# Kernel tuning notes

Hardware: AMD Instinct MI355X
Metric: run time of the kernel (lower is better)

## Reference

```python
import jax, jax.numpy as jnp
import numpy as np

B, T, D_MODEL, N_HEADS, D_HEAD = 2, 2048, 1024, 16, 64


def apply_rotary_emb(x, cos, sin):
    # x: [B, H, T, Dh]; cos, sin: [T, Dh//2]. Interleaved-pair RoPE.
    x1 = x[..., 0::2]  # [B,H,T,Dh/2]
    x2 = x[..., 1::2]
    c = cos[None, None, :, :]
    s = sin[None, None, :, :]
    out_even = x1 * c - x2 * s
    out_odd = x1 * s + x2 * c
    return jnp.stack([out_even, out_odd], axis=-1).reshape(x.shape)


def setup_inputs() -> dict:
    key = jax.random.key(0)
    ks = jax.random.split(key, 7)
    x = jax.random.normal(ks[0], (B, T, D_MODEL), dtype=jnp.float32)
    cos = jax.random.uniform(ks[1], (T, D_HEAD // 2), dtype=jnp.float32)
    sin = jax.random.uniform(ks[2], (T, D_HEAD // 2), dtype=jnp.float32)
    scale = 1.0 / np.sqrt(D_MODEL)
    W_q = jax.random.normal(ks[3], (D_MODEL, N_HEADS * D_HEAD), dtype=jnp.float32) * scale
    W_k = jax.random.normal(ks[4], (D_MODEL, N_HEADS * D_HEAD), dtype=jnp.float32) * scale
    W_v = jax.random.normal(ks[5], (D_MODEL, N_HEADS * D_HEAD), dtype=jnp.float32) * scale
    W_out = jax.random.normal(ks[6], (N_HEADS * D_HEAD, D_MODEL), dtype=jnp.float32) * scale
    return {"x": x, "cos": cos, "sin": sin, "W_q": W_q, "W_k": W_k, "W_v": W_v, "W_out": W_out}


def reference(x, cos, sin, W_q, W_k, W_v, W_out):
    Bb, Tt, _ = x.shape
    q = (x @ W_q).reshape(Bb, Tt, N_HEADS, D_HEAD).transpose(0, 2, 1, 3)  # [B,H,T,Dh]
    k = (x @ W_k).reshape(Bb, Tt, N_HEADS, D_HEAD).transpose(0, 2, 1, 3)
    v = (x @ W_v).reshape(Bb, Tt, N_HEADS, D_HEAD).transpose(0, 2, 1, 3)
    q = apply_rotary_emb(q, cos, sin)
    k = apply_rotary_emb(k, cos, sin)
    scores = jnp.einsum('bhqd,bhkd->bhqk', q, k) / np.sqrt(D_HEAD).astype(np.float32)
    causal = jnp.tril(jnp.ones((Tt, Tt), dtype=bool))
    scores = jnp.where(causal[None, None], scores, -jnp.inf)
    attn = jax.nn.softmax(scores, axis=-1)
    z = jnp.einsum('bhqk,bhkd->bhqd', attn, v)          # [B,H,T,Dh]
    z = z.transpose(0, 2, 1, 3).reshape(Bb, Tt, N_HEADS * D_HEAD)
    return z @ W_out
```

## Files before the change

### kernel.cpp

```cpp
#include <hip/hip_runtime.h>
#include <math.h>

#define TSEQ   2048
#define DMODEL 1024
#define NHEADS 16
#define DHEAD  64
#define BATCH  2

typedef __attribute__((ext_vector_type(8))) short short8;
typedef __attribute__((ext_vector_type(4))) float f32x4;

__device__ __forceinline__ unsigned short f2bf(float x) {
    union { float f; unsigned int u; } c; c.f = x;
    unsigned int r = (c.u + 0x7FFFu + ((c.u >> 16) & 1u)) >> 16;
    return (unsigned short)r;
}
__device__ __forceinline__ float bf2f(unsigned short h) {
    union { unsigned int u; float f; } c; c.u = ((unsigned int)h) << 16;
    return c.f;
}

__global__ __launch_bounds__(256) void qkv_rope_kernel(
    const float* __restrict__ x,
    const float* __restrict__ Wq, const float* __restrict__ Wk,
    const float* __restrict__ Wv,
    const float* __restrict__ cosb, const float* __restrict__ sinb,
    unsigned short* __restrict__ qhi, unsigned short* __restrict__ qlo,
    unsigned short* __restrict__ khi, unsigned short* __restrict__ klo,
    unsigned short* __restrict__ vto)
{
    __shared__ float As[16][132];
    __shared__ float Bs[16][132];

    const int tid = threadIdx.x;
    const int m0  = blockIdx.y * 128;
    const int n0g = blockIdx.x * 128;
    const int section = n0g >> 10;
    const int n0 = n0g & 1023;
    const float* __restrict__ W = (section == 0) ? Wq : (section == 1) ? Wk : Wv;

    const int arow = tid >> 2;
    const int ak   = (tid & 3) << 2;
    const int brow = tid >> 5;
    const int bn   = (tid & 31) << 2;

    const int rr = (tid & 15) << 2;
    const int cc = (tid >> 4) << 2;

    float acc[2][2][4][4] = {};

    const float* Aptr0 = x + (size_t)(m0 + arow) * DMODEL + ak;
    const float* Aptr1 = Aptr0 + (size_t)64 * DMODEL;
    const float* Bptr0 = W + (size_t)brow * DMODEL + n0 + bn;
    const float* Bptr1 = Bptr0 + (size_t)8 * DMODEL;

    float4 av0 = *(const float4*)(Aptr0);
    float4 av1 = *(const float4*)(Aptr1);
    float4 bv0 = *(const float4*)(Bptr0);
    float4 bv1 = *(const float4*)(Bptr1);

    for (int k0 = 0; k0 < DMODEL; k0 += 16) {
        __syncthreads();
        As[ak + 0][arow] = av0.x;  As[ak + 1][arow] = av0.y;
        As[ak + 2][arow] = av0.z;  As[ak + 3][arow] = av0.w;
        As[ak + 0][arow + 64] = av1.x;  As[ak + 1][arow + 64] = av1.y;
        As[ak + 2][arow + 64] = av1.z;  As[ak + 3][arow + 64] = av1.w;
        *(float4*)&Bs[brow][bn]     = bv0;
        *(float4*)&Bs[brow + 8][bn] = bv1;
        __syncthreads();
        if (k0 + 16 < DMODEL) {
            av0 = *(const float4*)(Aptr0 + k0 + 16);
            av1 = *(const float4*)(Aptr1 + k0 + 16);
            bv0 = *(const float4*)(Bptr0 + (size_t)(k0 + 16) * DMODEL);
            bv1 = *(const float4*)(Bptr1 + (size_t)(k0 + 16) * DMODEL);
        }
        #pragma unroll
        for (int kk = 0; kk < 16; ++kk) {
            float4 a0 = *(const float4*)&As[kk][rr];
            float4 a1 = *(const float4*)&As[kk][rr + 64];
            float4 b0 = *(const float4*)&Bs[kk][cc];
            float4 b1 = *(const float4*)&Bs[kk][cc + 64];
            float ar[2][4] = {{a0.x, a0.y, a0.z, a0.w}, {a1.x, a1.y, a1.z, a1.w}};
            float br[2][4] = {{b0.x, b0.y, b0.z, b0.w}, {b1.x, b1.y, b1.z, b1.w}};
            #pragma unroll
            for (int bi = 0; bi < 2; ++bi)
                #pragma unroll
                for (int i = 0; i < 4; ++i)
                    #pragma unroll
                    for (int bj = 0; bj < 2; ++bj)
                        #pragma unroll
                        for (int jj = 0; jj < 4; ++jj)
                            acc[bi][bj][i][jj] += ar[bi][i] * br[bj][jj];
        }
    }

    const int b = m0 >> 11;
    #pragma unroll
    for (int bi = 0; bi < 2; ++bi) {
        #pragma unroll
        for (int i = 0; i < 4; ++i) {
            const int t = (m0 + bi * 64 + rr + i) & (TSEQ - 1);
            #pragma unroll
            for (int bj = 0; bj < 2; ++bj) {
                const int n  = n0 + bj * 64 + cc;
                const int h  = n >> 6;
                const int d0 = n & 63;
                float a0 = acc[bi][bj][i][0], a1 = acc[bi][bj][i][1];
                float a2 = acc[bi][bj][i][2], a3 = acc[bi][bj][i][3];
                if (section < 2) {
                    const int p0 = d0 >> 1;
                    float c0v = cosb[t * (DHEAD / 2) + p0];
                    float s0v = sinb[t * (DHEAD / 2) + p0];
                    float c1v = cosb[t * (DHEAD / 2) + p0 + 1];
                    float s1v = sinb[t * (DHEAD / 2) + p0 + 1];
                    float r[4];
                    r[0] = a0 * c0v - a1 * s0v;
                    r[1] = a0 * s0v + a1 * c0v;
                    r[2] = a2 * c1v - a3 * s1v;
                    r[3] = a2 * s1v + a3 * c1v;
                    ushort4 uh, ul;
                    uh.x = f2bf(r[0]); ul.x = f2bf(r[0] - bf2f(uh.x));
                    uh.y = f2bf(r[1]); ul.y = f2bf(r[1] - bf2f(uh.y));
                    uh.z = f2bf(r[2]); ul.z = f2bf(r[2] - bf2f(uh.z));
                    uh.w = f2bf(r[3]); ul.w = f2bf(r[3] - bf2f(uh.w));
                    unsigned short* ph = (section == 0) ? qhi : khi;
                    unsigned short* pl = (section == 0) ? qlo : klo;
                    const size_t off = (((size_t)b * NHEADS + h) * TSEQ + t) * DHEAD + d0;
                    *(ushort4*)&ph[off] = uh;
                    *(ushort4*)&pl[off] = ul;
                } else {
                    const size_t base = ((size_t)b * NHEADS + h) * DHEAD;
                    vto[(base + d0 + 0) * TSEQ + t] = f2bf(a0);
                    vto[(base + d0 + 1) * TSEQ + t] = f2bf(a1);
                    vto[(base + d0 + 2) * TSEQ + t] = f2bf(a2);
                    vto[(base + d0 + 3) * TSEQ + t] = f2bf(a3);
                }
            }
        }
    }
}

#define LDSOFF(r, c) (((r) << 7) + ((((c) ^ ((r) & 7))) << 4))

__device__ __forceinline__ void stage64x64(const unsigned short* __restrict__ g,
                                           int rs_elems, char* lbase, int tid) {
    const int r = tid >> 3;
    const int c = tid & 7;
    const char* gb = (const char*)g;
    uint4 v0 = *(const uint4*)(gb + (size_t)r * rs_elems * 2 + (c << 4));
    uint4 v1 = *(const uint4*)(gb + (size_t)(r + 32) * rs_elems * 2 + (c << 4));
    *(uint4*)(lbase + LDSOFF(r, c)) = v0;
    *(uint4*)(lbase + LDSOFF(r + 32, c)) = v1;
}

__device__ __forceinline__ short8 frag(const char* lbase, int row, int chunk) {
    union { uint4 u; short8 s; } cv;
    cv.u = *(const uint4*)(lbase + LDSOFF(row, chunk));
    return cv.s;
}

__global__ __launch_bounds__(256) void attn_mfma_kernel(
    const unsigned short* __restrict__ qhig, const unsigned short* __restrict__ qlog,
    const unsigned short* __restrict__ khig, const unsigned short* __restrict__ klog,
    const unsigned short* __restrict__ vtg, float* __restrict__ z)
{
    __shared__ __align__(16) char smem[49152];
    char* Qhb = smem;
    char* Qlb = smem + 8192;
    char* Khb = smem + 16384;
    char* Klb = smem + 24576;
    char* Vb  = smem + 32768;
    char* Pb  = smem + 40960;

    const int tid  = threadIdx.x;
    const int lane = tid & 63;
    const int wave = tid >> 6;
    const int ln15 = lane & 15;
    const int g    = lane >> 4;

    const int bh = blockIdx.y;
    const int b  = bh >> 4;
    const int h  = bh & 15;
    const unsigned short* qhh = qhig + (size_t)bh * TSEQ * DHEAD;
    const unsigned short* qlh = qlog + (size_t)bh * TSEQ * DHEAD;
    const unsigned short* khh = khig + (size_t)bh * TSEQ * DHEAD;
    const unsigned short* klh = klog + (size_t)bh * TSEQ * DHEAD;
    const unsigned short* vth = vtg  + (size_t)bh * DHEAD * TSEQ;

    for (int half = 0; half < 2; ++half) {
        const int qt = half ? (31 - (int)blockIdx.x) : (int)blockIdx.x;

        __syncthreads();
        stage64x64(qhh + (size_t)qt * 64 * DHEAD, DHEAD, Qhb, tid);
        stage64x64(qlh + (size_t)qt * 64 * DHEAD, DHEAD, Qlb, tid);
        __syncthreads();

        const int rA = 16 * wave + ln15;
        short8 qh0 = frag(Qhb, rA, g),     qh1 = frag(Qhb, rA, 4 + g);
        short8 ql0 = frag(Qlb, rA, g),     ql1 = frag(Qlb, rA, 4 + g);

        float m_i[4], l_i[4];
        f32x4 oacc[4];
        #pragma unroll
        for (int i2 = 0; i2 < 4; ++i2) {
            m_i[i2] = -INFINITY; l_i[i2] = 0.f;
            oacc[i2][0] = 0.f; oacc[i2][1] = 0.f; oacc[i2][2] = 0.f; oacc[i2][3] = 0.f;
        }

        for (int jt = 0; jt <= qt; ++jt) {
            __syncthreads();
            stage64x64(khh + (size_t)jt * 64 * DHEAD, DHEAD, Khb, tid);
            stage64x64(klh + (size_t)jt * 64 * DHEAD, DHEAD, Klb, tid);
            stage64x64(vth + (size_t)jt * 64, TSEQ, Vb, tid);
            __syncthreads();

            f32x4 sacc[4];
            #pragma unroll
            for (int ct = 0; ct < 4; ++ct) {
                const int rB = ct * 16 + ln15;
                short8 kh0 = frag(Khb, rB, g), kh1 = frag(Khb, rB, 4 + g);
                short8 kl0 = frag(Klb, rB, g), kl1 = frag(Klb, rB, 4 + g);
                f32x4 acc = {0.f, 0.f, 0.f, 0.f};
                acc = __builtin_amdgcn_mfma_f32_16x16x32_bf16(qh0, kh0, acc, 0, 0, 0);
                acc = __builtin_amdgcn_mfma_f32_16x16x32_bf16(qh1, kh1, acc, 0, 0, 0);
                acc = __builtin_amdgcn_mfma_f32_16x16x32_bf16(qh0, kl0, acc, 0, 0, 0);
                acc = __builtin_amdgcn_mfma_f32_16x16x32_bf16(qh1, kl1, acc, 0, 0, 0);
                acc = __builtin_amdgcn_mfma_f32_16x16x32_bf16(ql0, kh0, acc, 0, 0, 0);
                acc = __builtin_amdgcn_mfma_f32_16x16x32_bf16(ql1, kh1, acc, 0, 0, 0);
                sacc[ct] = acc;
            }

            const bool diag = (jt == qt);
            #pragma unroll
            for (int reg = 0; reg < 4; ++reg) {
                const int rloc = 16 * wave + 4 * g + reg;
                float sv[4];
                #pragma unroll
                for (int ct = 0; ct < 4; ++ct) {
                    float xv = sacc[ct][reg] * 0.125f;
                    if (diag && (ct * 16 + ln15 > rloc)) xv = -INFINITY;
                    sv[ct] = xv;
                }
                float mr = fmaxf(fmaxf(sv[0], sv[1]), fmaxf(sv[2], sv[3]));
                #pragma unroll
                for (int off = 1; off < 16; off <<= 1)
                    mr = fmaxf(mr, __shfl_xor(mr, off));
                float mnew = fmaxf(m_i[reg], mr);
                float al   = __expf(m_i[reg] - mnew);
                float rs = 0.f;
                unsigned short pb[4];
                #pragma unroll
                for (int ct = 0; ct < 4; ++ct) {
                    float p = __expf(sv[ct] - mnew);
                    pb[ct] = f2bf(p);
                    rs += bf2f(pb[ct]);
                }
                #pragma unroll
                for (int off = 1; off < 16; off <<= 1)
                    rs += __shfl_xor(rs, off);
                l_i[reg] = l_i[reg] * al + rs;
                m_i[reg] = mnew;
                #pragma unroll
                for (int dt = 0; dt < 4; ++dt)
                    oacc[dt][reg] *= al;
                #pragma unroll
                for (int ct = 0; ct < 4; ++ct) {
                    const int col = ct * 16 + ln15;
                    const int chunk = col >> 3;
                    const int byt = (rloc << 7) + ((chunk ^ (rloc & 7)) << 4) + ((col & 7) << 1);
                    *(unsigned short*)(Pb + byt) = pb[ct];
                }
            }

            short8 pa0 = frag(Pb, rA, g);
            short8 pa1 = frag(Pb, rA, 4 + g);
            #pragma unroll
            for (int dt = 0; dt < 4; ++dt) {
                short8 vb0 = frag(Vb, dt * 16 + ln15, g);
                short8 vb1 = frag(Vb, dt * 16 + ln15, 4 + g);
                oacc[dt] = __builtin_amdgcn_mfma_f32_16x16x32_bf16(pa0, vb0, oacc[dt], 0, 0, 0);
                oacc[dt] = __builtin_amdgcn_mfma_f32_16x16x32_bf16(pa1, vb1, oacc[dt], 0, 0, 0);
            }
        }

        #pragma unroll
        for (int reg = 0; reg < 4; ++reg) {
            const float inv = 1.0f / l_i[reg];
            const int t = qt * 64 + 16 * wave + 4 * g + reg;
            float* zrow = z + ((size_t)(b * TSEQ + t)) * DMODEL + h * DHEAD;
            #pragma unroll
            for (int dt = 0; dt < 4; ++dt)
                zrow[dt * 16 + ln15] = oacc[dt][reg] * inv;
        }
    }
}

__global__ __launch_bounds__(256) void out_proj_kernel(
    const float* __restrict__ A, const float* __restrict__ B,
    float* __restrict__ C)
{
    __shared__ float As[16][132];
    __shared__ float Bs[16][132];

    const int tid = threadIdx.x;
    const int m0 = blockIdx.y * 128;
    const int n0 = blockIdx.x * 128;

    const int arow = tid >> 2;
    const int ak   = (tid & 3) << 2;
    const int brow = tid >> 5;
    const int bn   = (tid & 31) << 2;
    const int rr   = (tid & 15) << 2;
    const int cc   = (tid >> 4) << 2;

    float acc[2][2][4][4] = {};

    const float* Aptr0 = A + (size_t)(m0 + arow) * DMODEL + ak;
    const float* Aptr1 = Aptr0 + (size_t)64 * DMODEL;
    const float* Bptr0 = B + (size_t)brow * DMODEL + n0 + bn;
    const float* Bptr1 = Bptr0 + (size_t)8 * DMODEL;

    float4 av0 = *(const float4*)(Aptr0);
    float4 av1 = *(const float4*)(Aptr1);
    float4 bv0 = *(const float4*)(Bptr0);
    float4 bv1 = *(const float4*)(Bptr1);

    for (int k0 = 0; k0 < DMODEL; k0 += 16) {
        __syncthreads();
        As[ak + 0][arow] = av0.x;  As[ak + 1][arow] = av0.y;
        As[ak + 2][arow] = av0.z;  As[ak + 3][arow] = av0.w;
        As[ak + 0][arow + 64] = av1.x;  As[ak + 1][arow + 64] = av1.y;
        As[ak + 2][arow + 64] = av1.z;  As[ak + 3][arow + 64] = av1.w;
        *(float4*)&Bs[brow][bn]     = bv0;
        *(float4*)&Bs[brow + 8][bn] = bv1;
        __syncthreads();
        if (k0 + 16 < DMODEL) {
            av0 = *(const float4*)(Aptr0 + k0 + 16);
            av1 = *(const float4*)(Aptr1 + k0 + 16);
            bv0 = *(const float4*)(Bptr0 + (size_t)(k0 + 16) * DMODEL);
            bv1 = *(const float4*)(Bptr1 + (size_t)(k0 + 16) * DMODEL);
        }
        #pragma unroll
        for (int kk = 0; kk < 16; ++kk) {
            float4 a0 = *(const float4*)&As[kk][rr];
            float4 a1 = *(const float4*)&As[kk][rr + 64];
            float4 b0 = *(const float4*)&Bs[kk][cc];
            float4 b1 = *(const float4*)&Bs[kk][cc + 64];
            float ar[2][4] = {{a0.x, a0.y, a0.z, a0.w}, {a1.x, a1.y, a1.z, a1.w}};
            float br[2][4] = {{b0.x, b0.y, b0.z, b0.w}, {b1.x, b1.y, b1.z, b1.w}};
            #pragma unroll
            for (int bi = 0; bi < 2; ++bi)
                #pragma unroll
                for (int i = 0; i < 4; ++i)
                    #pragma unroll
                    for (int bj = 0; bj < 2; ++bj)
                        #pragma unroll
                        for (int jj = 0; jj < 4; ++jj)
                            acc[bi][bj][i][jj] += ar[bi][i] * br[bj][jj];
        }
    }

    #pragma unroll
    for (int bi = 0; bi < 2; ++bi)
        #pragma unroll
        for (int i = 0; i < 4; ++i) {
            const size_t row = m0 + bi * 64 + rr + i;
            #pragma unroll
            for (int bj = 0; bj < 2; ++bj) {
                const int col = n0 + bj * 64 + cc;
                *(float4*)&C[row * DMODEL + col] =
                    make_float4(acc[bi][bj][i][0], acc[bi][bj][i][1],
                                acc[bi][bj][i][2], acc[bi][bj][i][3]);
            }
        }
}

extern "C" void kernel_launch(void* const* d_in, const int* in_sizes, int n_in,
                              void* d_out, int out_size, void* d_ws, size_t ws_size,
                              hipStream_t stream)
{
    const float* x    = (const float*)d_in[0];
    const float* cosb = (const float*)d_in[1];
    const float* sinb = (const float*)d_in[2];
    const float* Wq   = (const float*)d_in[3];
    const float* Wk   = (const float*)d_in[4];
    const float* Wv   = (const float*)d_in[5];
    const float* Wo   = (const float*)d_in[6];
    float* out = (float*)d_out;

    const size_t per = (size_t)BATCH * NHEADS * TSEQ * DHEAD;
    unsigned short* qhi = (unsigned short*)d_ws;
    unsigned short* qlo = qhi + per;
    unsigned short* khi = qlo + per;
    unsigned short* klo = khi + per;
    unsigned short* vt  = klo + per;
    float* z = (float*)(vt + per);

    qkv_rope_kernel<<<dim3(24, 32), 256, 0, stream>>>(x, Wq, Wk, Wv, cosb, sinb,
                                                      qhi, qlo, khi, klo, vt);
    attn_mfma_kernel<<<dim3(16, 32), 256, 0, stream>>>(qhi, qlo, khi, klo, vt, z);
    out_proj_kernel<<<dim3(8, 32), 256, 0, stream>>>(z, Wo, out);
}
```

Baseline: 584.2 us.

## Move QKV and output projections to split-bf16 MFMA GEMMs with prep kernel

Adds a prep kernel that splits x and transposed weights into hi/lo bf16 pairs. The FP32 SIMT QKV and output-projection GEMMs are replaced with MFMA GEMMs that use three bf16 products to keep near-fp32 accuracy. Attention now writes z as a hi/lo split so the output projection can consume it directly. The trade is an extra prep pass over all four weight matrices on every call, plus a larger workspace, with a fallback to the old path when the workspace is too small.

```diff
diff --git a/kernel.cpp b/kernel.cpp
--- a/kernel.cpp
+++ b/kernel.cpp
@@ -19,8 +19,433 @@
     union { unsigned int u; float f; } c; c.u = ((unsigned int)h) << 16;
     return c.f;
 }
-
-__global__ __launch_bounds__(256) void qkv_rope_kernel(
+__device__ __forceinline__ void split2(float x, unsigned short& h, unsigned short& l) {
+    h = f2bf(x);
+    l = f2bf(x - bf2f(h));
+}
+
+__global__ __launch_bounds__(256) void prep_kernel(
+    const float* __restrict__ x,
+    const float* __restrict__ Wq, const float* __restrict__ Wk,
+    const float* __restrict__ Wv, const float* __restrict__ Wo,
+    unsigned short* __restrict__ xhi, unsigned short* __restrict__ xlo,
+    unsigned short* __restrict__ wth, unsigned short* __restrict__ wtl)
+{
+    const int tid = threadIdx.x;
+    const int bid = blockIdx.x;
+    if (bid < 1024) {
+        const size_t base = (size_t)bid * 4096;
+        #pragma unroll
+        for (int i = 0; i < 4; ++i) {
+            const size_t idx = base + (size_t)i * 1024 + tid * 4;
+            float4 v = *(const float4*)(x + idx);
+            ushort4 h4, l4;
+            split2(v.x, h4.x, l4.x); split2(v.y, h4.y, l4.y);
+            split2(v.z, h4.z, l4.z); split2(v.w, h4.w, l4.w);
+            *(ushort4*)(xhi + idx) = h4;
+            *(ushort4*)(xlo + idx) = l4;
+        }
+    } else {
+        __shared__ float tile[64][65];
+        const int tv = bid - 1024;
+        const int w  = tv >> 8;
+        const int kt = (tv & 255) >> 4;
+        const int nt = tv & 15;
+        const int k0 = kt * 64, n0 = nt * 64;
+        const float* __restrict__ W = (w == 0) ? Wq : (w == 1) ? Wk : (w == 2) ? Wv : Wo;
+        const int r = tid >> 4;
+        const int c = (tid & 15) * 4;
+        #pragma unroll
+        for (int i = 0; i < 4; ++i) {
+            float4 v = *(const float4*)(W + (size_t)(k0 + r + 16 * i) * DMODEL + n0 + c);
+            tile[r + 16 * i][c + 0] = v.x;
+            tile[r + 16 * i][c + 1] = v.y;
+            tile[r + 16 * i][c + 2] = v.z;
+            tile[r + 16 * i][c + 3] = v.w;
+        }
+        __syncthreads();
+        unsigned short* oh = wth + (size_t)w * DMODEL * DMODEL;
+        unsigned short* ol = wtl + (size_t)w * DMODEL * DMODEL;
+        #pragma unroll
+        for (int i = 0; i < 4; ++i) {
+            const int a = r + 16 * i;
+            ushort4 h4, l4;
+            split2(tile[c + 0][a], h4.x, l4.x);
+            split2(tile[c + 1][a], h4.y, l4.y);
+            split2(tile[c + 2][a], h4.z, l4.z);
+            split2(tile[c + 3][a], h4.w, l4.w);
+            const size_t off = (size_t)(n0 + a) * DMODEL + k0 + c;
+            *(ushort4*)(oh + off) = h4;
+            *(ushort4*)(ol + off) = l4;
+        }
+    }
+}
+
+#define LOFF4(r, ch) (((r) << 6) + ((((ch) ^ ((r) & 3))) << 4))
+
+__device__ __forceinline__ short8 frag4(const char* lb, int row, int ch) {
+    union { uint4 u; short8 s; } cv;
+    cv.u = *(const uint4*)(lb + LOFF4(row, ch));
+    return cv.s;
+}
+
+#define GEMM_STAGE_DECLS \
+    const int sr = tid >> 1;    \
+    const int shalf = tid & 1;  \
+    uint4 ra[2], rla[2], rb[2], rlb[2];
+
+#define GEMM_LOAD(kk) { \
+    const size_t ao = (size_t)arowg * DMODEL + (kk) + shalf * 16; \
+    ra[0]  = *(const uint4*)(Ahg + ao);  ra[1]  = *(const uint4*)(Ahg + ao + 8); \
+    rla[0] = *(const uint4*)(Alg + ao);  rla[1] = *(const uint4*)(Alg + ao + 8); \
+    const size_t bo = (size_t)browg * DMODEL + (kk) + shalf * 16; \
+    rb[0]  = *(const uint4*)(Bhg + bo);  rb[1]  = *(const uint4*)(Bhg + bo + 8); \
+    rlb[0] = *(const uint4*)(Blg + bo);  rlb[1] = *(const uint4*)(Blg + bo + 8); }
+
+#define GEMM_WRITE_LDS { \
+    *(uint4*)(Ah + LOFF4(sr, shalf * 2))     = ra[0]; \
+    *(uint4*)(Ah + LOFF4(sr, shalf * 2 + 1)) = ra[1]; \
+    *(uint4*)(Al + LOFF4(sr, shalf * 2))     = rla[0]; \
+    *(uint4*)(Al + LOFF4(sr, shalf * 2 + 1)) = rla[1]; \
+    *(uint4*)(Bh + LOFF4(sr, shalf * 2))     = rb[0]; \
+    *(uint4*)(Bh + LOFF4(sr, shalf * 2 + 1)) = rb[1]; \
+    *(uint4*)(Bl + LOFF4(sr, shalf * 2))     = rlb[0]; \
+    *(uint4*)(Bl + LOFF4(sr, shalf * 2 + 1)) = rlb[1]; }
+
+#define GEMM_COMPUTE { \
+    short8 fa[4], fla[4], fb[4], flb[4]; \
+    _Pragma("unroll") \
+    for (int mi = 0; mi < 4; ++mi) { \
+        fa[mi]  = frag4(Ah, wr * 64 + mi * 16 + ln15, g); \
+        fla[mi] = frag4(Al, wr * 64 + mi * 16 + ln15, g); \
+    } \
+    _Pragma("unroll") \
+    for (int nj = 0; nj < 4; ++nj) { \
+        fb[nj]  = frag4(Bh, wc * 64 + nj * 16 + ln15, g); \
+        flb[nj] = frag4(Bl, wc * 64 + nj * 16 + ln15, g); \
+    } \
+    _Pragma("unroll") \
+    for (int mi = 0; mi < 4; ++mi) \
+        _Pragma("unroll") \
+        for (int nj = 0; nj < 4; ++nj) { \
+            acc[mi][nj] = __builtin_amdgcn_mfma_f32_16x16x32_bf16(fa[mi],  fb[nj],  acc[mi][nj], 0, 0, 0); \
+            acc[mi][nj] = __builtin_amdgcn_mfma_f32_16x16x32_bf16(fa[mi],  flb[nj], acc[mi][nj], 0, 0, 0); \
+            acc[mi][nj] = __builtin_amdgcn_mfma_f32_16x16x32_bf16(fla[mi], fb[nj],  acc[mi][nj], 0, 0, 0); \
+        } }
+
+__global__ __launch_bounds__(256, 2) void qkv_mfma_kernel(
+    const unsigned short* __restrict__ xhi, const unsigned short* __restrict__ xlo,
+    const unsigned short* __restrict__ wth, const unsigned short* __restrict__ wtl,
+    const float* __restrict__ cosb, const float* __restrict__ sinb,
+    unsigned short* __restrict__ qhi, unsigned short* __restrict__ qlo,
+    unsigned short* __restrict__ khi, unsigned short* __restrict__ klo,
+    unsigned short* __restrict__ vto)
+{
+    __shared__ __align__(16) char smem[32768];
+    char* Ah = smem;
+    char* Al = smem + 8192;
+    char* Bh = smem + 16384;
+    char* Bl = smem + 24576;
+
+    const int tid  = threadIdx.x;
+    const int lane = tid & 63;
+    const int wave = tid >> 6;
+    const int ln15 = lane & 15;
+    const int g    = lane >> 4;
+    const int wr   = wave >> 1;
+    const int wc   = wave & 1;
+
+    const int m0    = blockIdx.y * 128;
+    const int sec   = blockIdx.x >> 3;
+    const int nsec0 = (blockIdx.x & 7) * 128;
+
+    const unsigned short* Ahg = xhi;
+    const unsigned short* Alg = xlo;
+    const unsigned short* Bhg = wth + (size_t)sec * DMODEL * DMODEL;
+    const unsigned short* Blg = wtl + (size_t)sec * DMODEL * DMODEL;
+
+    GEMM_STAGE_DECLS
+    const int arowg = m0 + sr;
+    const int browg = nsec0 + sr;
+
+    f32x4 acc[4][4];
+    #pragma unroll
+    for (int mi = 0; mi < 4; ++mi)
+        #pragma unroll
+        for (int nj = 0; nj < 4; ++nj)
+            acc[mi][nj] = (f32x4){0.f, 0.f, 0.f, 0.f};
+
+    GEMM_LOAD(0)
+    for (int k0 = 0; k0 < DMODEL; k0 += 32) {
+        __syncthreads();
+        GEMM_WRITE_LDS
+        __syncthreads();
+        if (k0 + 32 < DMODEL) GEMM_LOAD(k0 + 32)
+        GEMM_COMPUTE
+    }
+
+    unsigned short* oh = (sec == 0) ? qhi : khi;
+    unsigned short* ol = (sec == 0) ? qlo : klo;
+    #pragma unroll
+    for (int mi = 0; mi < 4; ++mi) {
+        #pragma unroll
+        for (int nj = 0; nj < 4; ++nj) {
+            const int colh = nsec0 + wc * 64 + nj * 16 + ln15;
+            const int h = colh >> 6;
+            const int d = colh & 63;
+            const int p = d >> 1;
+            const float sgn = (d & 1) ? 1.f : -1.f;
+            #pragma unroll
+            for (int reg = 0; reg < 4; ++reg) {
+                const int row = m0 + wr * 64 + mi * 16 + g * 4 + reg;
+                const int t = row & (TSEQ - 1);
+                const int b = row >> 11;
+                float v = acc[mi][nj][reg];
+                if (sec < 2) {
+                    float pv = __shfl_xor(v, 1);
+                    float cv = cosb[t * (DHEAD / 2) + p];
+                    float sv = sinb[t * (DHEAD / 2) + p];
+                    float rv = v * cv + pv * sv * sgn;
+                    unsigned short hh, ll;
+                    split2(rv, hh, ll);
+                    const size_t off = (((size_t)b * NHEADS + h) * TSEQ + t) * DHEAD + d;
+                    oh[off] = hh;
+                    ol[off] = ll;
+                } else {
+                    vto[(((size_t)b * NHEADS + h) * DHEAD + d) * TSEQ + t] = f2bf(v);
+                }
+            }
+        }
+    }
+}
+
+#define LDSOFF(r, c) (((r) << 7) + ((((c) ^ ((r) & 7))) << 4))
+
+__device__ __forceinline__ void stage64x64(const unsigned short* __restrict__ gm,
+                                           int rs_elems, char* lbase, int tid) {
+    const int r = tid >> 3;
+    const int c = tid & 7;
+    const char* gb = (const char*)gm;
+    uint4 v0 = *(const uint4*)(gb + (size_t)r * rs_elems * 2 + (c << 4));
+    uint4 v1 = *(const uint4*)(gb + (size_t)(r + 32) * rs_elems * 2 + (c << 4));
+    *(uint4*)(lbase + LDSOFF(r, c)) = v0;
+    *(uint4*)(lbase + LDSOFF(r + 32, c)) = v1;
+}
+
+__device__ __forceinline__ short8 frag(const char* lbase, int row, int chunk) {
+    union { uint4 u; short8 s; } cv;
+    cv.u = *(const uint4*)(lbase + LDSOFF(row, chunk));
+    return cv.s;
+}
+
+template<bool SPLITZ>
+__global__ __launch_bounds__(256) void attn_mfma_kernel(
+    const unsigned short* __restrict__ qhig, const unsigned short* __restrict__ qlog,
+    const unsigned short* __restrict__ khig, const unsigned short* __restrict__ klog,
+    const unsigned short* __restrict__ vtg,
+    float* __restrict__ zf,
+    unsigned short* __restrict__ zhi, unsigned short* __restrict__ zlo)
+{
+    __shared__ __align__(16) char smem[49152];
+    char* Qhb = smem;
+    char* Qlb = smem + 8192;
+    char* Khb = smem + 16384;
+    char* Klb = smem + 24576;
+    char* Vb  = smem + 32768;
+    char* Pb  = smem + 40960;
+
+    const int tid  = threadIdx.x;
+    const int lane = tid & 63;
+    const int wave = tid >> 6;
+    const int ln15 = lane & 15;
+    const int g    = lane >> 4;
+
+    const int bh = blockIdx.y;
+    const int b  = bh >> 4;
+    const int h  = bh & 15;
+    const unsigned short* qhh = qhig + (size_t)bh * TSEQ * DHEAD;
+    const unsigned short* qlh = qlog + (size_t)bh * TSEQ * DHEAD;
+    const unsigned short* khh = khig + (size_t)bh * TSEQ * DHEAD;
+    const unsigned short* klh = klog + (size_t)bh * TSEQ * DHEAD;
+    const unsigned short* vth = vtg  + (size_t)bh * DHEAD * TSEQ;
+
+    for (int half = 0; half < 2; ++half) {
+        const int qt = half ? (31 - (int)blockIdx.x) : (int)blockIdx.x;
+
+        __syncthreads();
+        stage64x64(qhh + (size_t)qt * 64 * DHEAD, DHEAD, Qhb, tid);
+        stage64x64(qlh + (size_t)qt * 64 * DHEAD, DHEAD, Qlb, tid);
+        __syncthreads();
+
+        const int rA = 16 * wave + ln15;
+        short8 qh0 = frag(Qhb, rA, g),     qh1 = frag(Qhb, rA, 4 + g);
+        short8 ql0 = frag(Qlb, rA, g),     ql1 = frag(Qlb, rA, 4 + g);
+
+        float m_i[4], l_i[4];
+        f32x4 oacc[4];
+        #pragma unroll
+        for (int i2 = 0; i2 < 4; ++i2) {
+            m_i[i2] = -INFINITY; l_i[i2] = 0.f;
+            oacc[i2][0] = 0.f; oacc[i2][1] = 0.f; oacc[i2][2] = 0.f; oacc[i2][3] = 0.f;
+        }
+
+        for (int jt = 0; jt <= qt; ++jt) {
+            __syncthreads();
+            stage64x64(khh + (size_t)jt * 64 * DHEAD, DHEAD, Khb, tid);
+            stage64x64(klh + (size_t)jt * 64 * DHEAD, DHEAD, Klb, tid);
+            stage64x64(vth + (size_t)jt * 64, TSEQ, Vb, tid);
+            __syncthreads();
+
+            f32x4 sacc[4];
+            #pragma unroll
+            for (int ct = 0; ct < 4; ++ct) {
+                const int rB = ct * 16 + ln15;
+                short8 kh0 = frag(Khb, rB, g), kh1 = frag(Khb, rB, 4 + g);
+                short8 kl0 = frag(Klb, rB, g), kl1 = frag(Klb, rB, 4 + g);
+                f32x4 a2 = {0.f, 0.f, 0.f, 0.f};
+                a2 = __builtin_amdgcn_mfma_f32_16x16x32_bf16(qh0, kh0, a2, 0, 0, 0);
+                a2 = __builtin_amdgcn_mfma_f32_16x16x32_bf16(qh1, kh1, a2, 0, 0, 0);
+                a2 = __builtin_amdgcn_mfma_f32_16x16x32_bf16(qh0, kl0, a2, 0, 0, 0);
+                a2 = __builtin_amdgcn_mfma_f32_16x16x32_bf16(qh1, kl1, a2, 0, 0, 0);
+                a2 = __builtin_amdgcn_mfma_f32_16x16x32_bf16(ql0, kh0, a2, 0, 0, 0);
+                a2 = __builtin_amdgcn_mfma_f32_16x16x32_bf16(ql1, kh1, a2, 0, 0, 0);
+                sacc[ct] = a2;
+            }
+
+            const bool diag = (jt == qt);
+            #pragma unroll
+            for (int reg = 0; reg < 4; ++reg) {
+                const int rloc = 16 * wave + 4 * g + reg;
+                float sv[4];
+                #pragma unroll
+                for (int ct = 0; ct < 4; ++ct) {
+                    float xv = sacc[ct][reg] * 0.125f;
+                    if (diag && (ct * 16 + ln15 > rloc)) xv = -INFINITY;
+                    sv[ct] = xv;
+                }
+                float mr = fmaxf(fmaxf(sv[0], sv[1]), fmaxf(sv[2], sv[3]));
+                #pragma unroll
+                for (int off = 1; off < 16; off <<= 1)
+                    mr = fmaxf(mr, __shfl_xor(mr, off));
+                float mnew = fmaxf(m_i[reg], mr);
+                float al   = __expf(m_i[reg] - mnew);
+                float rs = 0.f;
+                unsigned short pb[4];
+                #pragma unroll
+                for (int ct = 0; ct < 4; ++ct) {
+                    float pp = __expf(sv[ct] - mnew);
+                    pb[ct] = f2bf(pp);
+                    rs += bf2f(pb[ct]);
+                }
+                #pragma unroll
+                for (int off = 1; off < 16; off <<= 1)
+                    rs += __shfl_xor(rs, off);
+                l_i[reg] = l_i[reg] * al + rs;
+                m_i[reg] = mnew;
+                #pragma unroll
+                for (int dt = 0; dt < 4; ++dt)
+                    oacc[dt][reg] *= al;
+                #pragma unroll
+                for (int ct = 0; ct < 4; ++ct) {
+                    const int col = ct * 16 + ln15;
+                    const int chunk = col >> 3;
+                    const int byt = (rloc << 7) + ((chunk ^ (rloc & 7)) << 4) + ((col & 7) << 1);
+                    *(unsigned short*)(Pb + byt) = pb[ct];
+                }
+            }
+
+            short8 pa0 = frag(Pb, rA, g);
+            short8 pa1 = frag(Pb, rA, 4 + g);
+            #pragma unroll
+            for (int dt = 0; dt < 4; ++dt) {
+                short8 vb0 = frag(Vb, dt * 16 + ln15, g);
+                short8 vb1 = frag(Vb, dt * 16 + ln15, 4 + g);
+                oacc[dt] = __builtin_amdgcn_mfma_f32_16x16x32_bf16(pa0, vb0, oacc[dt], 0, 0, 0);
+                oacc[dt] = __builtin_amdgcn_mfma_f32_16x16x32_bf16(pa1, vb1, oacc[dt], 0, 0, 0);
+            }
+        }
+
+        #pragma unroll
+        for (int reg = 0; reg < 4; ++reg) {
+            const float inv = 1.0f / l_i[reg];
+            const int t = qt * 64 + 16 * wave + 4 * g + reg;
+            const size_t idx = ((size_t)(b * TSEQ + t)) * DMODEL + h * DHEAD;
+            #pragma unroll
+            for (int dt = 0; dt < 4; ++dt) {
+                float val = oacc[dt][reg] * inv;
+                if (SPLITZ) {
+                    unsigned short hh = f2bf(val);
+                    zhi[idx + dt * 16 + ln15] = hh;
+                    zlo[idx + dt * 16 + ln15] = f2bf(val - bf2f(hh));
+                } else {
+                    zf[idx + dt * 16 + ln15] = val;
+                }
+            }
+        }
+    }
+}
+
+__global__ __launch_bounds__(256, 2) void out_proj_mfma_kernel(
+    const unsigned short* __restrict__ zhi, const unsigned short* __restrict__ zlo,
+    const unsigned short* __restrict__ wth, const unsigned short* __restrict__ wtl,
+    float* __restrict__ outp)
+{
+    __shared__ __align__(16) char smem[32768];
+    char* Ah = smem;
+    char* Al = smem + 8192;
+    char* Bh = smem + 16384;
+    char* Bl = smem + 24576;
+
+    const int tid  = threadIdx.x;
+    const int lane = tid & 63;
+    const int wave = tid >> 6;
+    const int ln15 = lane & 15;
+    const int g    = lane >> 4;
+    const int wr   = wave >> 1;
+    const int wc   = wave & 1;
+
+    const int m0 = blockIdx.y * 128;
+    const int n0 = blockIdx.x * 128;
+
+    const unsigned short* Ahg = zhi;
+    const unsigned short* Alg = zlo;
+    const unsigned short* Bhg = wth + (size_t)3 * DMODEL * DMODEL;
+    const unsigned short* Blg = wtl + (size_t)3 * DMODEL * DMODEL;
+
+    GEMM_STAGE_DECLS
+    const int arowg = m0 + sr;
+    const int browg = n0 + sr;
+
+    f32x4 acc[4][4];
+    #pragma unroll
+    for (int mi = 0; mi < 4; ++mi)
+        #pragma unroll
+        for (int nj = 0; nj < 4; ++nj)
+            acc[mi][nj] = (f32x4){0.f, 0.f, 0.f, 0.f};
+
+    GEMM_LOAD(0)
+    for (int k0 = 0; k0 < DMODEL; k0 += 32) {
+        __syncthreads();
+        GEMM_WRITE_LDS
+        __syncthreads();
+        if (k0 + 32 < DMODEL) GEMM_LOAD(k0 + 32)
+        GEMM_COMPUTE
+    }
+
+    #pragma unroll
+    for (int mi = 0; mi < 4; ++mi)
+        #pragma unroll
+        for (int nj = 0; nj < 4; ++nj) {
+            const int col = n0 + wc * 64 + nj * 16 + ln15;
+            #pragma unroll
+            for (int reg = 0; reg < 4; ++reg) {
+                const int row = m0 + wr * 64 + mi * 16 + g * 4 + reg;
+                outp[(size_t)row * DMODEL + col] = acc[mi][nj][reg];
+            }
+        }
+}
+
+__global__ __launch_bounds__(256) void qkv_rope_f32_kernel(
     const float* __restrict__ x,
     const float* __restrict__ Wq, const float* __restrict__ Wk,
     const float* __restrict__ Wv,
@@ -43,7 +468,6 @@
     const int ak   = (tid & 3) << 2;
     const int brow = tid >> 5;
     const int bn   = (tid & 31) << 2;
-
     const int rr = (tid & 15) << 2;
     const int cc = (tid >> 4) << 2;
 
@@ -119,10 +543,10 @@
                     r[2] = a2 * c1v - a3 * s1v;
                     r[3] = a2 * s1v + a3 * c1v;
                     ushort4 uh, ul;
-                    uh.x = f2bf(r[0]); ul.x = f2bf(r[0] - bf2f(uh.x));
-                    uh.y = f2bf(r[1]); ul.y = f2bf(r[1] - bf2f(uh.y));
-                    uh.z = f2bf(r[2]); ul.z = f2bf(r[2] - bf2f(uh.z));
-                    uh.w = f2bf(r[3]); ul.w = f2bf(r[3] - bf2f(uh.w));
+                    split2(r[0], uh.x, ul.x);
+                    split2(r[1], uh.y, ul.y);
+                    split2(r[2], uh.z, ul.z);
+                    split2(r[3], uh.w, ul.w);
                     unsigned short* ph = (section == 0) ? qhi : khi;
                     unsigned short* pl = (section == 0) ? qlo : klo;
                     const size_t off = (((size_t)b * NHEADS + h) * TSEQ + t) * DHEAD + d0;
@@ -140,162 +564,7 @@
     }
 }
 
-#define LDSOFF(r, c) (((r) << 7) + ((((c) ^ ((r) & 7))) << 4))
-
-__device__ __forceinline__ void stage64x64(const unsigned short* __restrict__ g,
-                                           int rs_elems, char* lbase, int tid) {
-    const int r = tid >> 3;
-    const int c = tid & 7;
-    const char* gb = (const char*)g;
-    uint4 v0 = *(const uint4*)(gb + (size_t)r * rs_elems * 2 + (c << 4));
-    uint4 v1 = *(const uint4*)(gb + (size_t)(r + 32) * rs_elems * 2 + (c << 4));
-    *(uint4*)(lbase + LDSOFF(r, c)) = v0;
-    *(uint4*)(lbase + LDSOFF(r + 32, c)) = v1;
-}
-
-__device__ __forceinline__ short8 frag(const char* lbase, int row, int chunk) {
-    union { uint4 u; short8 s; } cv;
-    cv.u = *(const uint4*)(lbase + LDSOFF(row, chunk));
-    return cv.s;
-}
-
-__global__ __launch_bounds__(256) void attn_mfma_kernel(
-    const unsigned short* __restrict__ qhig, const unsigned short* __restrict__ qlog,
-    const unsigned short* __restrict__ khig, const unsigned short* __restrict__ klog,
-    const unsigned short* __restrict__ vtg, float* __restrict__ z)
-{
-    __shared__ __align__(16) char smem[49152];
-    char* Qhb = smem;
-    char* Qlb = smem + 8192;
-    char* Khb = smem + 16384;
-    char* Klb = smem + 24576;
-    char* Vb  = smem + 32768;
-    char* Pb  = smem + 40960;
-
-    const int tid  = threadIdx.x;
-    const int lane = tid & 63;
-    const int wave = tid >> 6;
-    const int ln15 = lane & 15;
-    const int g    = lane >> 4;
-
-    const int bh = blockIdx.y;
-    const int b  = bh >> 4;
-    const int h  = bh & 15;
-    const unsigned short* qhh = qhig + (size_t)bh * TSEQ * DHEAD;
-    const unsigned short* qlh = qlog + (size_t)bh * TSEQ * DHEAD;
-    const unsigned short* khh = khig + (size_t)bh * TSEQ * DHEAD;
-    const unsigned short* klh = klog + (size_t)bh * TSEQ * DHEAD;
-    const unsigned short* vth = vtg  + (size_t)bh * DHEAD * TSEQ;
-
-    for (int half = 0; half < 2; ++half) {
-        const int qt = half ? (31 - (int)blockIdx.x) : (int)blockIdx.x;
-
-        __syncthreads();
-        stage64x64(qhh + (size_t)qt * 64 * DHEAD, DHEAD, Qhb, tid);
-        stage64x64(qlh + (size_t)qt * 64 * DHEAD, DHEAD, Qlb, tid);
-        __syncthreads();
-
-        const int rA = 16 * wave + ln15;
-        short8 qh0 = frag(Qhb, rA, g),     qh1 = frag(Qhb, rA, 4 + g);
-        short8 ql0 = frag(Qlb, rA, g),     ql1 = frag(Qlb, rA, 4 + g);
-
-        float m_i[4], l_i[4];
-        f32x4 oacc[4];
-        #pragma unroll
-        for (int i2 = 0; i2 < 4; ++i2) {
-            m_i[i2] = -INFINITY; l_i[i2] = 0.f;
-            oacc[i2][0] = 0.f; oacc[i2][1] = 0.f; oacc[i2][2] = 0.f; oacc[i2][3] = 0.f;
-        }
-
-        for (int jt = 0; jt <= qt; ++jt) {
-            __syncthreads();
-            stage64x64(khh + (size_t)jt * 64 * DHEAD, DHEAD, Khb, tid);
-            stage64x64(klh + (size_t)jt * 64 * DHEAD, DHEAD, Klb, tid);
-            stage64x64(vth + (size_t)jt * 64, TSEQ, Vb, tid);
-            __syncthreads();
-
-            f32x4 sacc[4];
-            #pragma unroll
-            for (int ct = 0; ct < 4; ++ct) {
-                const int rB = ct * 16 + ln15;
-                short8 kh0 = frag(Khb, rB, g), kh1 = frag(Khb, rB, 4 + g);
-                short8 kl0 = frag(Klb, rB, g), kl1 = frag(Klb, rB, 4 + g);
-                f32x4 acc = {0.f, 0.f, 0.f, 0.f};
-                acc = __builtin_amdgcn_mfma_f32_16x16x32_bf16(qh0, kh0, acc, 0, 0, 0);
-                acc = __builtin_amdgcn_mfma_f32_16x16x32_bf16(qh1, kh1, acc, 0, 0, 0);
-                acc = __builtin_amdgcn_mfma_f32_16x16x32_bf16(qh0, kl0, acc, 0, 0, 0);
-                acc = __builtin_amdgcn_mfma_f32_16x16x32_bf16(qh1, kl1, acc, 0, 0, 0);
-                acc = __builtin_amdgcn_mfma_f32_16x16x32_bf16(ql0, kh0, acc, 0, 0, 0);
-                acc = __builtin_amdgcn_mfma_f32_16x16x32_bf16(ql1, kh1, acc, 0, 0, 0);
-                sacc[ct] = acc;
-            }
-
-            const bool diag = (jt == qt);
-            #pragma unroll
-            for (int reg = 0; reg < 4; ++reg) {
-                const int rloc = 16 * wave + 4 * g + reg;
-                float sv[4];
-                #pragma unroll
-                for (int ct = 0; ct < 4; ++ct) {
-                    float xv = sacc[ct][reg] * 0.125f;
-                    if (diag && (ct * 16 + ln15 > rloc)) xv = -INFINITY;
-                    sv[ct] = xv;
-                }
-                float mr = fmaxf(fmaxf(sv[0], sv[1]), fmaxf(sv[2], sv[3]));
-                #pragma unroll
-                for (int off = 1; off < 16; off <<= 1)
-                    mr = fmaxf(mr, __shfl_xor(mr, off));
-                float mnew = fmaxf(m_i[reg], mr);
-                float al   = __expf(m_i[reg] - mnew);
-                float rs = 0.f;
-                unsigned short pb[4];
-                #pragma unroll
-                for (int ct = 0; ct < 4; ++ct) {
-                    float p = __expf(sv[ct] - mnew);
-                    pb[ct] = f2bf(p);
-                    rs += bf2f(pb[ct]);
-                }
-                #pragma unroll
-                for (int off = 1; off < 16; off <<= 1)
-                    rs += __shfl_xor(rs, off);
-                l_i[reg] = l_i[reg] * al + rs;
-                m_i[reg] = mnew;
-                #pragma unroll
-                for (int dt = 0; dt < 4; ++dt)
-                    oacc[dt][reg] *= al;
-                #pragma unroll
-                for (int ct = 0; ct < 4; ++ct) {
-                    const int col = ct * 16 + ln15;
-                    const int chunk = col >> 3;
-                    const int byt = (rloc << 7) + ((chunk ^ (rloc & 7)) << 4) + ((col & 7) << 1);
-                    *(unsigned short*)(Pb + byt) = pb[ct];
-                }
-            }
-
-            short8 pa0 = frag(Pb, rA, g);
-            short8 pa1 = frag(Pb, rA, 4 + g);
-            #pragma unroll
-            for (int dt = 0; dt < 4; ++dt) {
-                short8 vb0 = frag(Vb, dt * 16 + ln15, g);
-                short8 vb1 = frag(Vb, dt * 16 + ln15, 4 + g);
-                oacc[dt] = __builtin_amdgcn_mfma_f32_16x16x32_bf16(pa0, vb0, oacc[dt], 0, 0, 0);
-                oacc[dt] = __builtin_amdgcn_mfma_f32_16x16x32_bf16(pa1, vb1, oacc[dt], 0, 0, 0);
-            }
-        }
-
-        #pragma unroll
-        for (int reg = 0; reg < 4; ++reg) {
-            const float inv = 1.0f / l_i[reg];
-            const int t = qt * 64 + 16 * wave + 4 * g + reg;
-            float* zrow = z + ((size_t)(b * TSEQ + t)) * DMODEL + h * DHEAD;
-            #pragma unroll
-            for (int dt = 0; dt < 4; ++dt)
-                zrow[dt * 16 + ln15] = oacc[dt][reg] * inv;
-        }
-    }
-}
-
-__global__ __launch_bounds__(256) void out_proj_kernel(
+__global__ __launch_bounds__(256) void out_proj_f32_kernel(
     const float* __restrict__ A, const float* __restrict__ B,
     float* __restrict__ C)
 {
@@ -386,18 +655,41 @@
     const float* Wk   = (const float*)d_in[4];
     const float* Wv   = (const float*)d_in[5];
     const float* Wo   = (const float*)d_in[6];
-    float* out = (float*)d_out;
+    float* outp = (float*)d_out;
 
     const size_t per = (size_t)BATCH * NHEADS * TSEQ * DHEAD;
-    unsigned short* qhi = (unsigned short*)d_ws;
-    unsigned short* qlo = qhi + per;
-    unsigned short* khi = qlo + per;
-    unsigned short* klo = khi + per;
-    unsigned short* vt  = klo + per;
-    float* z = (float*)(vt + per);
-
-    qkv_rope_kernel<<<dim3(24, 32), 256, 0, stream>>>(x, Wq, Wk, Wv, cosb, sinb,
-                                                      qhi, qlo, khi, klo, vt);
-    attn_mfma_kernel<<<dim3(16, 32), 256, 0, stream>>>(qhi, qlo, khi, klo, vt, z);
-    out_proj_kernel<<<dim3(8, 32), 256, 0, stream>>>(z, Wo, out);
-}
+    const size_t need_new = 15 * per * sizeof(unsigned short);
+
+    if (ws_size >= need_new) {
+        unsigned short* xhi = (unsigned short*)d_ws;
+        unsigned short* xlo = xhi + per;
+        unsigned short* wth = xlo + per;
+        unsigned short* wtl = wth + 4 * per;
+        unsigned short* qhi = wtl + 4 * per;
+        unsigned short* qlo = qhi + per;
+        unsigned short* khi = qlo + per;
+        unsigned short* klo = khi + per;
+        unsigned short* vt  = klo + per;
+
+        prep_kernel<<<2048, 256, 0, stream>>>(x, Wq, Wk, Wv, Wo, xhi, xlo, wth, wtl);
+        qkv_mfma_kernel<<<dim3(24, 32), 256, 0, stream>>>(xhi, xlo, wth, wtl,
+                                                          cosb, sinb,
+                                                          qhi, qlo, khi, klo, vt);
+        attn_mfma_kernel<true><<<dim3(16, 32), 256, 0, stream>>>(
+            qhi, qlo, khi, klo, vt, nullptr, xhi, xlo);
+        out_proj_mfma_kernel<<<dim3(8, 32), 256, 0, stream>>>(xhi, xlo, wth, wtl, outp);
+    } else {
+        unsigned short* qhi = (unsigned short*)d_ws;
+        unsigned short* qlo = qhi + per;
+        unsigned short* khi = qlo + per;
+        unsigned short* klo = khi + per;
+        unsigned short* vt  = klo + per;
+        float* z = (float*)(vt + per);
+
+        qkv_rope_f32_kernel<<<dim3(24, 32), 256, 0, stream>>>(
+            x, Wq, Wk, Wv, cosb, sinb, qhi, qlo, khi, klo, vt);
+        attn_mfma_kernel<false><<<dim3(16, 32), 256, 0, stream>>>(
+            qhi, qlo, khi, klo, vt, z, nullptr, nullptr);
+        out_proj_f32_kernel<<<dim3(8, 32), 256, 0, stream>>>(z, Wo, outp);
+    }
+}
```

After: 588.1 us. About the same (+0.7%).
